# Performance work log

Hardware: AMD Instinct MI355X
Metric: run time of the kernel (lower is better)

The kernel has to match this reference:

```python
import jax, jax.numpy as jnp
import numpy as np

# Topology constants (fixed DAG ontology)
B = 16384          # batch
IN_DIM = 4096      # input_dim
N_LEAF = 64        # leaf terms with direct input maps
IPL = 64           # inputs per leaf (disjoint slices; one-hot connection mask -> diag weights)
N_MID = 16         # mid-level modules
CPM = 4            # leaf children per mid module
MID_N = 128        # neurons per mid module
OUT = 256          # output_dim at root


def setup_inputs() -> dict:
    key = jax.random.key(0)
    k = jax.random.split(key, 7)
    return {
        "x": jax.random.normal(k[0], (B, IN_DIM), jnp.float32),
        # input-layer kernels: only the masked diagonal entries of each [IN_DIM, IPL]
        # kernel are nonzero after kernel*connections, so store them as [N_LEAF, IPL]
        "w_inp": jax.random.normal(k[1], (N_LEAF, IPL), jnp.float32) * 0.1,
        "pbias": jnp.ones((N_LEAF,), jnp.float32),  # pbias=1.0 per input layer
        "W_mid": jax.random.normal(k[2], (N_MID, CPM * IPL, MID_N), jnp.float32) * 0.05,
        "b_mid": jnp.zeros((N_MID, MID_N), jnp.float32),
        "W_root": jax.random.normal(k[3], (N_MID * MID_N, OUT), jnp.float32) * 0.05,
        "b_root": jnp.zeros((OUT,), jnp.float32),
    }


def reference(x, w_inp, pbias, W_mid, b_mid, W_root, b_root):
    b = x.shape[0]
    # Leaf input layers: gather each leaf's input slice, multiply by its diagonal
    # kernel entries (== dot(x, kernel*one_hot_mask)), linear act, add pbias.
    leaf = x.reshape(b, N_LEAF, IPL) * w_inp + pbias[:, None]          # [B, N_LEAF, IPL]
    # Mid modules: concat CPM leaf children -> masked-dense (mask all ones) + bias + tanh
    mid_in = leaf.reshape(b, N_MID, CPM * IPL)                          # [B, N_MID, 256]
    mid = jnp.tanh(jnp.einsum('bgi,gio->bgo', mid_in, W_mid) + b_mid)   # [B, N_MID, 128]
    # Root module: concat all mid children -> dense + bias, linear output activation
    out = mid.reshape(b, N_MID * MID_N) @ W_root + b_root               # [B, OUT]
    return out
```

## Files before the change

kernel.cpp:

```cpp
#include <hip/hip_runtime.h>

typedef __attribute__((ext_vector_type(8))) short short8;
typedef __attribute__((ext_vector_type(4))) float floatx4;
typedef unsigned short ushort_t;
typedef unsigned int uint32;


__device__ __forceinline__ uint32 f2bf_bits(float f) {
  uint32 u = __builtin_bit_cast(uint32, f);
  u += 0x7fffu + ((u >> 16) & 1u);
  return u >> 16;
}

__device__ __forceinline__ float tanh_fast(float x) {
  float e = __expf(2.0f * x);
  return 1.0f - 2.0f * __builtin_amdgcn_rcpf(e + 1.0f);
}

#define MFMA16(a, b, c) __builtin_amdgcn_mfma_f32_16x16x32_bf16((a), (b), (c), 0, 0, 0)

#define BAR_LGKM() asm volatile("s_waitcnt lgkmcnt(0)\n\ts_barrier" ::: "memory")


__global__ __launch_bounds__(256) void prep(const float* __restrict__ w_inp,
                                            const float* __restrict__ pbias,
                                            const float* __restrict__ W_mid,
                                            const float* __restrict__ b_mid,
                                            const float* __restrict__ W_root,
                                            ushort_t* __restrict__ Wtm2,
                                            ushort_t* __restrict__ Wtr2,
                                            float* __restrict__ bias_eff) {
  __shared__ float tl[32][33];
  __shared__ float red[256];
  const int b = blockIdx.x, t = threadIdx.x;
  const int tx = t & 31, ty = t >> 5;

  if (b < 512) {
    const int g = b >> 5, tile = b & 31;
    const int i0 = (tile >> 2) * 32, o0 = (tile & 3) * 32;
#pragma unroll
    for (int r = 0; r < 4; ++r) {
      const int il = ty * 4 + r;
      tl[il][tx] = W_mid[(g << 15) + (i0 + il) * 128 + o0 + tx] * w_inp[g * 256 + i0 + il];
    }
    __syncthreads();
    const int nl = t >> 3, s = t & 7;
    const int o = o0 + nl, nb = o >> 4, l15 = o & 15;
    const int kk = i0 >> 5;
    const int iloc = s * 4, kh = iloc >> 3, e0 = iloc & 7;
    const uint32 lo = (uint32)f2bf_bits(tl[iloc + 0][nl]) |
                      ((uint32)f2bf_bits(tl[iloc + 1][nl]) << 16);
    const uint32 hi = (uint32)f2bf_bits(tl[iloc + 2][nl]) |
                      ((uint32)f2bf_bits(tl[iloc + 3][nl]) << 16);
    uint2* dst = (uint2*)(Wtm2 + (size_t)(((g * 8 + nb) * 8 + kk) * 512 + kh * 128 + l15 * 8 + e0));
    *dst = make_uint2(lo, hi);
  } else if (b < 1024) {
    const int bb = b - 512;
    const int k0 = (bb >> 3) * 32, o0 = (bb & 7) * 32;
#pragma unroll
    for (int r = 0; r < 4; ++r) {
      const int kl = ty * 4 + r;
      tl[kl][tx] = W_root[(k0 + kl) * 256 + o0 + tx];
    }
    __syncthreads();
    const int nl = t >> 3, s = t & 7;
    const int o = o0 + nl, nb = o >> 4, l15 = o & 15;
    const int g = k0 >> 7, kk2 = (k0 >> 5) & 3;
    const int iloc = s * 4, kh = iloc >> 3, e0 = iloc & 7;
    const uint32 lo = (uint32)f2bf_bits(tl[iloc + 0][nl]) |
                      ((uint32)f2bf_bits(tl[iloc + 1][nl]) << 16);
    const uint32 hi = (uint32)f2bf_bits(tl[iloc + 2][nl]) |
                      ((uint32)f2bf_bits(tl[iloc + 3][nl]) << 16);
    uint2* dst = (uint2*)(Wtr2 + (size_t)(((g * 16 + nb) * 4 + kk2) * 512 + kh * 128 + l15 * 8 + e0));
    *dst = make_uint2(lo, hi);
  } else {
    const int g = b - 1024;
    const int o = t & 127, ih = t >> 7;
    const float* wp = W_mid + (g << 15) + ih * 128 * 128 + o;
    const float pb0 = pbias[g * 4 + ih * 2];
    const float pb1 = pbias[g * 4 + ih * 2 + 1];
    float s = 0.f;
#pragma unroll 8
    for (int ii = 0; ii < 128; ++ii) s += (ii < 64 ? pb0 : pb1) * wp[ii * 128];
    red[t] = s;
    __syncthreads();
    if (ih == 0) bias_eff[g * 128 + o] = b_mid[g * 128 + o] + red[o] + red[128 + o];
  }
}


template <bool SPLIT>
__global__ __launch_bounds__(256, 3) void fused(const float* __restrict__ x,
                                                const ushort_t* __restrict__ Wtm2,
                                                const ushort_t* __restrict__ Wtr2,
                                                const float* __restrict__ bias_eff,
                                                const float* __restrict__ b_root,
                                                float* __restrict__ dst) {
  constexpr int GROUPS = SPLIT ? 8 : 16;

  __shared__ __align__(16) ushort_t sX[32 * 264];
  __shared__ __align__(16) ushort_t sMid[32 * 136];

  const int t = threadIdx.x;
  const int lane = t & 63;
  const int wv = __builtin_amdgcn_readfirstlane(t >> 6);
  const int tile = SPLIT ? (int)(blockIdx.x >> 1) : (int)blockIdx.x;
  const int h = SPLIT ? (int)(blockIdx.x & 1) : 0;
  const int G0 = h * 8;
  const int m0 = tile * 32;
  const int l15 = lane & 15;
  const int kh = lane >> 4;

  const int xr = t >> 3, xq = t & 7;
  const float* xbase = x + (size_t)(m0 + xr) * 4096 + (size_t)G0 * 256 + xq * 4;
  uint32* sxw = (uint32*)(sX + xr * 264 + xq * 4);

  const ushort_t* sxa0 = sX + l15 * 264 + kh * 8;
  const ushort_t* sxa1 = sX + (16 + l15) * 264 + kh * 8;
  const ushort_t* sma0 = sMid + l15 * 136 + kh * 8;
  const ushort_t* sma1 = sMid + (16 + l15) * 136 + kh * 8;

  const ushort_t* wtm_base = Wtm2 + (((size_t)G0) << 15) + (size_t)wv * (2 * 8 * 512) + (size_t)lane * 8;
  const ushort_t* wtr_base = Wtr2 + (((size_t)G0) << 15) + (size_t)wv * (4 * 4 * 512) + (size_t)lane * 8;

  float4 rx[8];
  floatx4 racc[2][4] = {};

#pragma unroll
  for (int p = 0; p < 8; ++p) rx[p] = *(const float4*)(xbase + p * 32);

#pragma unroll 1
  for (int g = 0; g < GROUPS; ++g) {
    const ushort_t* wb0 = wtm_base + ((size_t)g << 15);
    const ushort_t* wb1 = wb0 + 4096;
    short8 mb[2][2];
    mb[0][0] = *(const short8*)(wb0);
    mb[0][1] = *(const short8*)(wb1);
    mb[1][0] = *(const short8*)(wb0 + 512);
    mb[1][1] = *(const short8*)(wb1 + 512);
    const float bias0 = bias_eff[(G0 + g) * 128 + wv * 32 + l15];
    const float bias1 = bias_eff[(G0 + g) * 128 + wv * 32 + 16 + l15];

#pragma unroll
    for (int p = 0; p < 8; ++p) {
      uint32 bx = __builtin_bit_cast(uint32, rx[p].x) + 0x8000u;
      uint32 by = __builtin_bit_cast(uint32, rx[p].y) + 0x8000u;
      uint32 bz = __builtin_bit_cast(uint32, rx[p].z) + 0x8000u;
      uint32 bw = __builtin_bit_cast(uint32, rx[p].w) + 0x8000u;
      uint32 lo = __builtin_amdgcn_perm(by, bx, 0x07060302u);
      uint32 hi = __builtin_amdgcn_perm(bw, bz, 0x07060302u);
      *(uint2*)(sxw + p * 16) = make_uint2(lo, hi);
    }

    BAR_LGKM();

    floatx4 macc[2][2] = {};
#pragma unroll
    for (int kk = 0; kk < 8; ++kk) {
      short8 a0 = *(const short8*)(sxa0 + kk * 32);
      short8 a1 = *(const short8*)(sxa1 + kk * 32);
      short8 b0 = mb[kk & 1][0], b1 = mb[kk & 1][1];
      if (kk < 6) {
        mb[kk & 1][0] = *(const short8*)(wb0 + (kk + 2) * 512);
        mb[kk & 1][1] = *(const short8*)(wb1 + (kk + 2) * 512);
      }
      macc[0][0] = MFMA16(a0, b0, macc[0][0]);
      macc[0][1] = MFMA16(a0, b1, macc[0][1]);
      macc[1][0] = MFMA16(a1, b0, macc[1][0]);
      macc[1][1] = MFMA16(a1, b1, macc[1][1]);
    }

    const ushort_t* wb = wtr_base + ((size_t)g << 15);
    short8 rb[2][4];
#pragma unroll
    for (int ni = 0; ni < 4; ++ni) rb[0][ni] = *(const short8*)(wb + (ni * 4 + 0) * 512);
#pragma unroll
    for (int ni = 0; ni < 4; ++ni) rb[1][ni] = *(const short8*)(wb + (ni * 4 + 1) * 512);

    __builtin_amdgcn_sched_barrier(0);

    if (g < GROUPS - 1) {
      const float* xn = xbase + (g + 1) * 256;
#pragma unroll
      for (int p = 0; p < 8; ++p) rx[p] = *(const float4*)(xn + p * 32);
    }

    __builtin_amdgcn_sched_barrier(0);

#pragma unroll
    for (int ni = 0; ni < 2; ++ni) {
      const float bias = ni ? bias1 : bias0;
      const int col = wv * 32 + ni * 16 + l15;
#pragma unroll
      for (int mi = 0; mi < 2; ++mi)
#pragma unroll
        for (int r = 0; r < 4; ++r) {
          const int row = mi * 16 + kh * 4 + r;
          sMid[row * 136 + col] = (ushort_t)f2bf_bits(tanh_fast(macc[mi][ni][r] + bias));
        }
    }

    BAR_LGKM();

#pragma unroll
    for (int kk2 = 0; kk2 < 4; ++kk2) {
      short8 a0 = *(const short8*)(sma0 + kk2 * 32);
      short8 a1 = *(const short8*)(sma1 + kk2 * 32);
      short8 b0 = rb[kk2 & 1][0], b1 = rb[kk2 & 1][1];
      short8 b2 = rb[kk2 & 1][2], b3 = rb[kk2 & 1][3];
      if (kk2 < 2) {
#pragma unroll
        for (int ni = 0; ni < 4; ++ni)
          rb[kk2 & 1][ni] = *(const short8*)(wb + (ni * 4 + kk2 + 2) * 512);
      }
      racc[0][0] = MFMA16(a0, b0, racc[0][0]);
      racc[0][1] = MFMA16(a0, b1, racc[0][1]);
      racc[0][2] = MFMA16(a0, b2, racc[0][2]);
      racc[0][3] = MFMA16(a0, b3, racc[0][3]);
      racc[1][0] = MFMA16(a1, b0, racc[1][0]);
      racc[1][1] = MFMA16(a1, b1, racc[1][1]);
      racc[1][2] = MFMA16(a1, b2, racc[1][2]);
      racc[1][3] = MFMA16(a1, b3, racc[1][3]);
    }
  }

  float* o = SPLIT ? dst + (size_t)h * (16384 * 256) : dst;
#pragma unroll
  for (int ni = 0; ni < 4; ++ni) {
    const int col = wv * 64 + ni * 16 + l15;
    const float br = SPLIT ? 0.0f : b_root[col];
#pragma unroll
    for (int mi = 0; mi < 2; ++mi)
#pragma unroll
      for (int r = 0; r < 4; ++r) {
        const int row = m0 + mi * 16 + kh * 4 + r;
        o[(size_t)row * 256 + col] = racc[mi][ni][r] + br;
      }
  }
}


__global__ __launch_bounds__(256) void reducek(const float* __restrict__ part,
                                               const float* __restrict__ b_root,
                                               float* __restrict__ out) {
  const int i = blockIdx.x * 256 + threadIdx.x;
  float4 a = ((const float4*)part)[i];
  float4 c = ((const float4*)(part + (size_t)16384 * 256))[i];
  float4 br = ((const float4*)b_root)[i & 63];
  float4 r;
  r.x = a.x + c.x + br.x;
  r.y = a.y + c.y + br.y;
  r.z = a.z + c.z + br.z;
  r.w = a.w + c.w + br.w;
  ((float4*)out)[i] = r;
}


extern "C" void kernel_launch(void* const* d_in, const int* in_sizes, int n_in,
                              void* d_out, int out_size, void* d_ws, size_t ws_size,
                              hipStream_t stream) {
  const float* x      = (const float*)d_in[0];
  const float* w_inp  = (const float*)d_in[1];
  const float* pbias  = (const float*)d_in[2];
  const float* W_mid  = (const float*)d_in[3];
  const float* b_mid  = (const float*)d_in[4];
  const float* W_root = (const float*)d_in[5];
  const float* b_root = (const float*)d_in[6];
  float* out = (float*)d_out;

  char* ws = (char*)d_ws;
  ushort_t* Wtm2     = (ushort_t*)(ws);
  ushort_t* Wtr2     = (ushort_t*)(ws + (1 << 20));
  float*    bias_eff = (float*)   (ws + (2 << 20));
  float*    part     = (float*)   (ws + (4 << 20));

  const size_t need = (size_t)(4 << 20) + 2ull * 16384 * 256 * 4;
  const bool split = ws_size >= need;

  prep<<<dim3(1040), dim3(256), 0, stream>>>(w_inp, pbias, W_mid, b_mid, W_root, Wtm2, Wtr2, bias_eff);
  if (split) {
    fused<true><<<dim3(1024), dim3(256), 0, stream>>>(x, Wtm2, Wtr2, bias_eff, b_root, part);
    reducek<<<dim3(4096), dim3(256), 0, stream>>>(part, b_root, out);
  } else {
    fused<false><<<dim3(512), dim3(256), 0, stream>>>(x, Wtm2, Wtr2, bias_eff, b_root, out);
  }
}
```

Baseline: 398.7 us.

## Enlarge fused tile to 64 rows with 512-thread blocks and 8 waves

Doubles the row tile per block from 32 to 64 and the block size from 256 to 512 threads, so eight waves each own a narrower slice of output columns while sharing the larger staged input tile. Each wave now loads half as many mid and root weight fragments and reuses each one across four row fragments instead of two. The goal is to cut global weight traffic per output row and improve MFMA reuse. In exchange LDS use per block doubles, the grid is halved, and occupancy per CU may change under the new launch bounds.

Result: faster. 388.5 us (-2.6%).

```diff
diff --git a/kernel.cpp b/kernel.cpp
--- a/kernel.cpp
+++ b/kernel.cpp
@@ -90,7 +90,7 @@
 
 
 template <bool SPLIT>
-__global__ __launch_bounds__(256, 3) void fused(const float* __restrict__ x,
+__global__ __launch_bounds__(512, 4) void fused(const float* __restrict__ x,
                                                 const ushort_t* __restrict__ Wtm2,
                                                 const ushort_t* __restrict__ Wtr2,
                                                 const float* __restrict__ bias_eff,
@@ -98,16 +98,16 @@
                                                 float* __restrict__ dst) {
   constexpr int GROUPS = SPLIT ? 8 : 16;
 
-  __shared__ __align__(16) ushort_t sX[32 * 264];
-  __shared__ __align__(16) ushort_t sMid[32 * 136];
+  __shared__ __align__(16) ushort_t sX[64 * 264];
+  __shared__ __align__(16) ushort_t sMid[64 * 136];
 
   const int t = threadIdx.x;
   const int lane = t & 63;
-  const int wv = __builtin_amdgcn_readfirstlane(t >> 6);
+  const int w = __builtin_amdgcn_readfirstlane(t >> 6);
   const int tile = SPLIT ? (int)(blockIdx.x >> 1) : (int)blockIdx.x;
   const int h = SPLIT ? (int)(blockIdx.x & 1) : 0;
   const int G0 = h * 8;
-  const int m0 = tile * 32;
+  const int m0 = tile * 64;
   const int l15 = lane & 15;
   const int kh = lane >> 4;
 
@@ -115,16 +115,19 @@
   const float* xbase = x + (size_t)(m0 + xr) * 4096 + (size_t)G0 * 256 + xq * 4;
   uint32* sxw = (uint32*)(sX + xr * 264 + xq * 4);
 
-  const ushort_t* sxa0 = sX + l15 * 264 + kh * 8;
-  const ushort_t* sxa1 = sX + (16 + l15) * 264 + kh * 8;
-  const ushort_t* sma0 = sMid + l15 * 136 + kh * 8;
-  const ushort_t* sma1 = sMid + (16 + l15) * 136 + kh * 8;
-
-  const ushort_t* wtm_base = Wtm2 + (((size_t)G0) << 15) + (size_t)wv * (2 * 8 * 512) + (size_t)lane * 8;
-  const ushort_t* wtr_base = Wtr2 + (((size_t)G0) << 15) + (size_t)wv * (4 * 4 * 512) + (size_t)lane * 8;
+  const ushort_t* sxa[4];
+  const ushort_t* sma[4];
+#pragma unroll
+  for (int af = 0; af < 4; ++af) {
+    sxa[af] = sX + (af * 16 + l15) * 264 + kh * 8;
+    sma[af] = sMid + (af * 16 + l15) * 136 + kh * 8;
+  }
+
+  const ushort_t* wtm_base = Wtm2 + (((size_t)G0) << 15) + (size_t)w * (8 * 512) + (size_t)lane * 8;
+  const ushort_t* wtr_base = Wtr2 + (((size_t)G0) << 15) + (size_t)w * (2 * 4 * 512) + (size_t)lane * 8;
 
   float4 rx[8];
-  floatx4 racc[2][4] = {};
+  floatx4 racc[4][2] = {};
 
 #pragma unroll
   for (int p = 0; p < 8; ++p) rx[p] = *(const float4*)(xbase + p * 32);
@@ -132,14 +135,10 @@
 #pragma unroll 1
   for (int g = 0; g < GROUPS; ++g) {
     const ushort_t* wb0 = wtm_base + ((size_t)g << 15);
-    const ushort_t* wb1 = wb0 + 4096;
-    short8 mb[2][2];
-    mb[0][0] = *(const short8*)(wb0);
-    mb[0][1] = *(const short8*)(wb1);
-    mb[1][0] = *(const short8*)(wb0 + 512);
-    mb[1][1] = *(const short8*)(wb1 + 512);
-    const float bias0 = bias_eff[(G0 + g) * 128 + wv * 32 + l15];
-    const float bias1 = bias_eff[(G0 + g) * 128 + wv * 32 + 16 + l15];
+    short8 mb[2];
+    mb[0] = *(const short8*)(wb0);
+    mb[1] = *(const short8*)(wb0 + 512);
+    const float bias = bias_eff[(G0 + g) * 128 + w * 16 + l15];
 
 #pragma unroll
     for (int p = 0; p < 8; ++p) {
@@ -154,28 +153,27 @@
 
     BAR_LGKM();
 
-    floatx4 macc[2][2] = {};
+    floatx4 macc[4] = {};
 #pragma unroll
     for (int kk = 0; kk < 8; ++kk) {
-      short8 a0 = *(const short8*)(sxa0 + kk * 32);
-      short8 a1 = *(const short8*)(sxa1 + kk * 32);
-      short8 b0 = mb[kk & 1][0], b1 = mb[kk & 1][1];
-      if (kk < 6) {
-        mb[kk & 1][0] = *(const short8*)(wb0 + (kk + 2) * 512);
-        mb[kk & 1][1] = *(const short8*)(wb1 + (kk + 2) * 512);
-      }
-      macc[0][0] = MFMA16(a0, b0, macc[0][0]);
-      macc[0][1] = MFMA16(a0, b1, macc[0][1]);
-      macc[1][0] = MFMA16(a1, b0, macc[1][0]);
-      macc[1][1] = MFMA16(a1, b1, macc[1][1]);
+      short8 a0 = *(const short8*)(sxa[0] + kk * 32);
+      short8 a1 = *(const short8*)(sxa[1] + kk * 32);
+      short8 a2 = *(const short8*)(sxa[2] + kk * 32);
+      short8 a3 = *(const short8*)(sxa[3] + kk * 32);
+      short8 b = mb[kk & 1];
+      if (kk < 6) mb[kk & 1] = *(const short8*)(wb0 + (kk + 2) * 512);
+      macc[0] = MFMA16(a0, b, macc[0]);
+      macc[1] = MFMA16(a1, b, macc[1]);
+      macc[2] = MFMA16(a2, b, macc[2]);
+      macc[3] = MFMA16(a3, b, macc[3]);
     }
 
     const ushort_t* wb = wtr_base + ((size_t)g << 15);
-    short8 rb[2][4];
-#pragma unroll
-    for (int ni = 0; ni < 4; ++ni) rb[0][ni] = *(const short8*)(wb + (ni * 4 + 0) * 512);
-#pragma unroll
-    for (int ni = 0; ni < 4; ++ni) rb[1][ni] = *(const short8*)(wb + (ni * 4 + 1) * 512);
+    short8 rb[2][2];
+#pragma unroll
+    for (int ni = 0; ni < 2; ++ni) rb[0][ni] = *(const short8*)(wb + (ni * 4 + 0) * 512);
+#pragma unroll
+    for (int ni = 0; ni < 2; ++ni) rb[1][ni] = *(const short8*)(wb + (ni * 4 + 1) * 512);
 
     __builtin_amdgcn_sched_barrier(0);
 
@@ -187,16 +185,14 @@
 
     __builtin_amdgcn_sched_barrier(0);
 
-#pragma unroll
-    for (int ni = 0; ni < 2; ++ni) {
-      const float bias = ni ? bias1 : bias0;
-      const int col = wv * 32 + ni * 16 + l15;
-#pragma unroll
-      for (int mi = 0; mi < 2; ++mi)
+    {
+      const int col = w * 16 + l15;
+#pragma unroll
+      for (int af = 0; af < 4; ++af)
 #pragma unroll
         for (int r = 0; r < 4; ++r) {
-          const int row = mi * 16 + kh * 4 + r;
-          sMid[row * 136 + col] = (ushort_t)f2bf_bits(tanh_fast(macc[mi][ni][r] + bias));
+          const int row = af * 16 + kh * 4 + r;
+          sMid[row * 136 + col] = (ushort_t)f2bf_bits(tanh_fast(macc[af][r] + bias));
         }
     }
 
@@ -204,37 +200,38 @@
 
 #pragma unroll
     for (int kk2 = 0; kk2 < 4; ++kk2) {
-      short8 a0 = *(const short8*)(sma0 + kk2 * 32);
-      short8 a1 = *(const short8*)(sma1 + kk2 * 32);
+      short8 a0 = *(const short8*)(sma[0] + kk2 * 32);
+      short8 a1 = *(const short8*)(sma[1] + kk2 * 32);
+      short8 a2 = *(const short8*)(sma[2] + kk2 * 32);
+      short8 a3 = *(const short8*)(sma[3] + kk2 * 32);
       short8 b0 = rb[kk2 & 1][0], b1 = rb[kk2 & 1][1];
-      short8 b2 = rb[kk2 & 1][2], b3 = rb[kk2 & 1][3];
       if (kk2 < 2) {
 #pragma unroll
-        for (int ni = 0; ni < 4; ++ni)
+        for (int ni = 0; ni < 2; ++ni)
           rb[kk2 & 1][ni] = *(const short8*)(wb + (ni * 4 + kk2 + 2) * 512);
       }
       racc[0][0] = MFMA16(a0, b0, racc[0][0]);
       racc[0][1] = MFMA16(a0, b1, racc[0][1]);
-      racc[0][2] = MFMA16(a0, b2, racc[0][2]);
-      racc[0][3] = MFMA16(a0, b3, racc[0][3]);
       racc[1][0] = MFMA16(a1, b0, racc[1][0]);
       racc[1][1] = MFMA16(a1, b1, racc[1][1]);
-      racc[1][2] = MFMA16(a1, b2, racc[1][2]);
-      racc[1][3] = MFMA16(a1, b3, racc[1][3]);
+      racc[2][0] = MFMA16(a2, b0, racc[2][0]);
+      racc[2][1] = MFMA16(a2, b1, racc[2][1]);
+      racc[3][0] = MFMA16(a3, b0, racc[3][0]);
+      racc[3][1] = MFMA16(a3, b1, racc[3][1]);
     }
   }
 
   float* o = SPLIT ? dst + (size_t)h * (16384 * 256) : dst;
 #pragma unroll
-  for (int ni = 0; ni < 4; ++ni) {
-    const int col = wv * 64 + ni * 16 + l15;
+  for (int ni = 0; ni < 2; ++ni) {
+    const int col = w * 32 + ni * 16 + l15;
     const float br = SPLIT ? 0.0f : b_root[col];
 #pragma unroll
-    for (int mi = 0; mi < 2; ++mi)
+    for (int af = 0; af < 4; ++af)
 #pragma unroll
       for (int r = 0; r < 4; ++r) {
-        const int row = m0 + mi * 16 + kh * 4 + r;
-        o[(size_t)row * 256 + col] = racc[mi][ni][r] + br;
+        const int row = m0 + af * 16 + kh * 4 + r;
+        o[(size_t)row * 256 + col] = racc[af][ni][r] + br;
       }
   }
 }
@@ -279,9 +276,9 @@
 
   prep<<<dim3(1040), dim3(256), 0, stream>>>(w_inp, pbias, W_mid, b_mid, W_root, Wtm2, Wtr2, bias_eff);
   if (split) {
-    fused<true><<<dim3(1024), dim3(256), 0, stream>>>(x, Wtm2, Wtr2, bias_eff, b_root, part);
+    fused<true><<<dim3(512), dim3(512), 0, stream>>>(x, Wtm2, Wtr2, bias_eff, b_root, part);
     reducek<<<dim3(4096), dim3(256), 0, stream>>>(part, b_root, out);
   } else {
-    fused<false><<<dim3(512), dim3(256), 0, stream>>>(x, Wtm2, Wtr2, bias_eff, b_root, out);
-  }
-}
+    fused<false><<<dim3(256), dim3(512), 0, stream>>>(x, Wtm2, Wtr2, bias_eff, b_root, out);
+  }
+}
```
